# Performance work log

Hardware: AMD Instinct MI355X
Metric: run time of the kernel (lower is better)

The kernel has to match this reference:

```python
import jax, jax.numpy as jnp
import numpy as np


def conv(x, w, b=None, pad=1):
    y = jax.lax.conv_general_dilated(x, w, (1, 1), [(pad, pad), (pad, pad)],
                                     dimension_numbers=('NCHW', 'OIHW', 'NCHW'))
    if b is not None:
        y = y + b[None, :, None, None]
    return y


def grid_sample(img, gx, gy):
    # bilinear, zeros padding, align_corners=False (torch F.grid_sample default)
    B, C, H, W = img.shape
    ix = ((gx + 1.0) * W - 1.0) * 0.5
    iy = ((gy + 1.0) * H - 1.0) * 0.5
    x0 = jnp.floor(ix)
    y0 = jnp.floor(iy)

    def gather(xi, yi):
        valid = (xi >= 0) & (xi <= W - 1) & (yi >= 0) & (yi <= H - 1)
        xc = jnp.clip(xi, 0, W - 1).astype(jnp.int32)
        yc = jnp.clip(yi, 0, H - 1).astype(jnp.int32)
        b = jnp.arange(B)[:, None, None]
        return img[b, :, yc, xc] * valid[..., None].astype(img.dtype)  # (B,H,W,C)

    wx1 = ix - x0
    wy1 = iy - y0
    wx0 = 1.0 - wx1
    wy0 = 1.0 - wy1
    out = (gather(x0, y0) * (wx0 * wy0)[..., None]
           + gather(x0 + 1, y0) * (wx1 * wy0)[..., None]
           + gather(x0, y0 + 1) * (wx0 * wy1)[..., None]
           + gather(x0 + 1, y0 + 1) * (wx1 * wy1)[..., None])
    return out.transpose(0, 3, 1, 2)  # (B,C,H,W)


def setup_inputs() -> dict:
    key = jax.random.key(0)
    ks = jax.random.split(key, 32)
    B, H, W, hd = 4, 512, 512, 16
    f = lambda k, shp: jax.random.normal(k, shp, dtype=jnp.float32) * 0.05
    z = lambda n: jnp.zeros((n,), dtype=jnp.float32)
    d = {
        'net': f(ks[0], (B, hd, H, W)),
        'inp': f(ks[1], (B, hd, H, W)),
        'corr': f(ks[2], (B, 3, H, W)),
        'noise': f(ks[3], (B, 3, H, W)),
        # BasicMotionEncoder (channels=3, hidden=32, output_dim=64)
        'wc1': f(ks[4], (32, 3, 3, 3)), 'bc1': z(32),
        'wc2': f(ks[5], (32, 32, 3, 3)), 'bc2': z(32),
        'wf1': f(ks[6], (32, 3, 3, 3)), 'bf1': z(32),
        'wf2': f(ks[7], (32, 32, 3, 3)), 'bf2': z(32),
        'we': f(ks[8], (61, 64, 3, 3)), 'be': z(61),
        # SepConvGRU (hidden_size=16, L=4)
        'loc1_w': f(ks[9], (16, 96, 5, 5)), 'loc1_b': z(16),
        'loc2_w': f(ks[10], (8, 16, 5, 5)), 'loc2_b': z(8),
        'wz': f(ks[11], (16, 144, 3, 3)), 'bz': z(16),
        'wr': f(ks[12], (16, 144, 3, 3)), 'br': z(16),
        'wq': f(ks[13], (16, 96, 3, 3)), 'bq': z(16),
        # CBAM (reduction 16 -> mid=1; bias-free, standard impl)
        'ca_w1': f(ks[14], (1, 16, 1, 1)),
        'ca_w2': f(ks[15], (16, 1, 1, 1)),
        'sa_w': f(ks[16], (1, 2, 7, 7)),
        # FlowHead (input 16, hidden 64, out 3)
        'fh1_w': f(ks[17], (64, 16, 3, 3)), 'fh1_b': z(64),
        'fh2_w': f(ks[18], (3, 64, 3, 3)), 'fh2_b': z(3),
    }
    return d


def reference(net, inp, corr, noise, wc1, bc1, wc2, bc2, wf1, bf1, wf2, bf2, we, be,
              loc1_w, loc1_b, loc2_w, loc2_b, wz, bz, wr, br, wq, bq,
              ca_w1, ca_w2, sa_w, fh1_w, fh1_b, fh2_w, fh2_b):
    # --- BasicMotionEncoder ---
    cor = jax.nn.relu(conv(corr, wc1, bc1, 1))
    cor = jax.nn.relu(conv(cor, wc2, bc2, 1))
    flo = jax.nn.relu(conv(noise, wf1, bf1, 1))
    flo = jax.nn.relu(conv(flo, wf2, bf2, 1))
    mo = jax.nn.relu(conv(jnp.concatenate([cor, flo], 1), we, be, 1))
    motion = jnp.concatenate([mo, noise], 1)  # (B,64,H,W)
    x = jnp.concatenate([inp, motion], 1)     # (B,hd+64,H,W)
    h = net
    B, C, H, W = h.shape
    # --- SepConvGRU ---
    t = jax.nn.leaky_relu(conv(jnp.concatenate([x, h], 1), loc1_w, loc1_b, 2), 0.2)
    flows = conv(t, loc2_w, loc2_b, 2)        # (B,2L,H,W)
    L = flows.shape[1] // 2
    flows = flows.reshape(B, L, 2, H, W)
    xx = jnp.arange(W, dtype=h.dtype)[None, None, :]  # (1,1,W)
    yy = jnp.arange(H, dtype=h.dtype)[None, :, None]  # (1,H,1)

    def warp_one(flow):  # flow: (B,2,H,W); warp h by -flow
        vgx = xx - flow[:, 0]
        vgy = yy - flow[:, 1]
        gx = 2.0 * vgx / max(W - 1, 1) - 1.0
        gy = 2.0 * vgy / max(H - 1, 1) - 1.0
        return grid_sample(h, gx, gy)

    wrapped = jax.vmap(warp_one, in_axes=1, out_axes=1)(flows)  # (B,L,C,H,W)
    wrapped = wrapped.reshape(B, L * C, H, W)
    hx = jnp.concatenate([wrapped, x], 1)     # (B,9*hd,H,W)
    zg = jax.nn.sigmoid(conv(hx, wz, bz, 1))
    rg = jax.nn.sigmoid(conv(hx, wr, br, 1))
    q = jnp.tanh(conv(jnp.concatenate([rg * h, x], 1), wq, bq, 1))
    h = (1.0 - zg) * h + zg * q
    # --- CBAM ---
    avg = h.mean((2, 3), keepdims=True)
    mx = h.max((2, 3), keepdims=True)
    mlp = lambda v: conv(jax.nn.relu(conv(v, ca_w1, None, 0)), ca_w2, None, 0)
    h = h * jax.nn.sigmoid(mlp(avg) + mlp(mx))
    sa = jnp.concatenate([h.mean(1, keepdims=True), h.max(1, keepdims=True)], 1)
    h = h * jax.nn.sigmoid(conv(sa, sa_w, None, 3))
    # --- FlowHead ---
    delta_flow = conv(jax.nn.relu(conv(h, fh1_w, fh1_b, 1)), fh2_w, fh2_b, 1)
    return h, delta_flow
```

## Files before the change

### kernel.cpp

```cpp
#include <hip/hip_runtime.h>
#include <hip/hip_bf16.h>
#include <math.h>

using bf16 = __hip_bfloat16;
typedef __attribute__((ext_vector_type(8))) short short8;
typedef __attribute__((ext_vector_type(4))) float f32x4;

__device__ __forceinline__ float b2f(bf16 v){ return __bfloat162float(v); }
__device__ __forceinline__ bf16 f2b(float v){ return __float2bfloat16(v); }
__device__ __forceinline__ float bs2f(short s){
  union{unsigned u; float f;} x; x.u = ((unsigned)(unsigned short)s)<<16; return x.f;
}

template<int A> __device__ __forceinline__ float act_fn(float v){
  if constexpr (A==1) return fmaxf(v, 0.f);
  else if constexpr (A==2) return v > 0.f ? v : 0.2f*v;
  else if constexpr (A==3) return 1.f/(1.f+expf(-v));
  else if constexpr (A==4) return tanhf(v);
  else return v;
}

struct Srcs9 { const bf16* p[9]; int code[9]; };

template<int KK, int ACT, int NT>
__global__ __launch_bounds__(256) void conv_mfma(
    Srcs9 S, int Gin, const bf16* __restrict__ flows,
    const bf16* __restrict__ Bw, const float* __restrict__ bias,
    bf16* __restrict__ outS, size_t slabS, float* __restrict__ outF, int Cout,
    int H, int W)
{
  constexpr int TS=16, HALO=TS+KK-1, PAD=KK/2, NPAIR=(KK*KK+1)/2, HH=HALO*HALO;
  constexpr int NMT = (NT==1)?4:((NT==2)?8:16);
  __shared__ __align__(16) bf16 As[2][HH*24];
  const int tid=threadIdx.x, lane=tid&63, wv=tid>>6;
  const int ln=lane&15, gq=lane>>4;
  const int tilesx=W/TS;
  const int tx0=(blockIdx.x%tilesx)*TS, ty0=(blockIdx.x/tilesx)*TS;
  const int b=blockIdx.z; const int HW=H*W;
  int ntile, mt0;
  if constexpr (NT==1){ ntile=0;    mt0=wv*4; }
  else if constexpr (NT==2){ ntile=wv&1; mt0=(wv>>1)*8; }
  else { ntile=wv; mt0=0; }

  f32x4 acc[NMT];
  #pragma unroll
  for (int t=0;t<NMT;++t) acc[t]=(f32x4){0.f,0.f,0.f,0.f};

  const short8 Z8 = {0,0,0,0,0,0,0,0};
  const int px0=tid, px1=tid+256;
  const int hy0=px0/HALO, hx0=px0-hy0*HALO;
  const int hy1=px1/HALO, hx1=px1-hy1*HALO;
  const bool act1 = (px1<HH);
  const int gy0=ty0+hy0-PAD, gx0=tx0+hx0-PAD;
  const int gy1=ty0+hy1-PAD, gx1=tx0+hx1-PAD;
  const bool in0 = (gy0>=0&&gy0<H&&gx0>=0&&gx0<W);
  const bool in1 = act1 && (gy1>=0&&gy1<H&&gx1>=0&&gx1<W);
  const size_t po0 = ((size_t)b*HW + (size_t)(in0?gy0:0)*W + (in0?gx0:0))*16;
  const size_t po1 = ((size_t)b*HW + (size_t)(in1?gy1:0)*W + (in1?gx1:0))*16;

  auto gather = [&](int g, bool inb, size_t po, int gy, int gx, short8& A0, short8& A1){
    const int code = S.code[g];
    const bf16* sp = S.p[g];
    if (code == 0) {
      if (inb) {
        const bf16* qp = sp + po;
        A0 = *(const short8*)qp; A1 = *(const short8*)(qp+8);
      } else { A0 = Z8; A1 = Z8; }
    } else {
      if (inb) {
        const int l = code-1;
        const unsigned fp_ = *(const unsigned*)(flows + po + 2*l);
        const float fx = bs2f((short)(fp_&0xffff)), fy = bs2f((short)(fp_>>16));
        const float vgx = (float)gx - fx, vgy = (float)gy - fy;
        const float gxn = 2.f*vgx/(float)(W-1) - 1.f;
        const float gyn = 2.f*vgy/(float)(H-1) - 1.f;
        const float ix = ((gxn+1.f)*(float)W - 1.f)*0.5f;
        const float iy = ((gyn+1.f)*(float)H - 1.f)*0.5f;
        const float x0f = floorf(ix), y0f = floorf(iy);
        const float wx1 = ix-x0f, wy1 = iy-y0f, wx0 = 1.f-wx1, wy0 = 1.f-wy1;
        const int x0=(int)x0f, y0=(int)y0f, x1=x0+1, y1=y0+1;
        const bool vx0=(x0>=0)&(x0<W), vx1=(x1>=0)&(x1<W);
        const bool vy0=(y0>=0)&(y0<H), vy1=(y1>=0)&(y1<H);
        const int xc0=min(max(x0,0),W-1), xc1=min(max(x1,0),W-1);
        const int yc0=min(max(y0,0),H-1), yc1=min(max(y1,0),H-1);
        const float w00=wx0*wy0*((vx0&&vy0)?1.f:0.f);
        const float w10=wx1*wy0*((vx1&&vy0)?1.f:0.f);
        const float w01=wx0*wy1*((vx0&&vy1)?1.f:0.f);
        const float w11=wx1*wy1*((vx1&&vy1)?1.f:0.f);
        const bf16* nb = sp + (size_t)b*HW*16;
        const bf16* p00 = nb + ((size_t)yc0*W+xc0)*16;
        const bf16* p10 = nb + ((size_t)yc0*W+xc1)*16;
        const bf16* p01 = nb + ((size_t)yc1*W+xc0)*16;
        const bf16* p11 = nb + ((size_t)yc1*W+xc1)*16;
        const short8 a00=*(const short8*)p00, b00=*(const short8*)(p00+8);
        const short8 a10=*(const short8*)p10, b10=*(const short8*)(p10+8);
        const short8 a01=*(const short8*)p01, b01=*(const short8*)(p01+8);
        const short8 a11=*(const short8*)p11, b11=*(const short8*)(p11+8);
        __align__(16) bf16 tmp[16];
        #pragma unroll
        for (int c=0;c<8;++c){
          tmp[c]   = f2b(w00*bs2f(a00[c]) + w10*bs2f(a10[c]) + w01*bs2f(a01[c]) + w11*bs2f(a11[c]));
          tmp[8+c] = f2b(w00*bs2f(b00[c]) + w10*bs2f(b10[c]) + w01*bs2f(b01[c]) + w11*bs2f(b11[c]));
        }
        A0 = *(const short8*)tmp; A1 = *(const short8*)(tmp+8);
      } else { A0 = Z8; A1 = Z8; }
    }
  };

  auto mfma_g = [&](int g, const char* bufc){
    const bf16* bw = Bw + ((size_t)g*NPAIR*NT + ntile)*512;
    const char* bufm = bufc + (size_t)mt0*(HALO*48);
    #pragma unroll
    for (int p=0;p<NPAIR;++p){
      const short8 bfrag = *(const short8*)(bw + (size_t)p*(NT*512) + lane*8);
      int off = 2*p + (gq>>1);
      if (off >= KK*KK) off = 0;
      const int dy = off/KK, dx = off - (off/KK)*KK;
      const int ce = (dy*HALO + ln + dx)*48 + ((gq&1)<<4);
      #pragma unroll
      for (int t=0;t<NMT;++t){
        const short8 af = *(const short8*)(bufm + (size_t)t*(HALO*48) + ce);
        acc[t] = __builtin_amdgcn_mfma_f32_16x16x32_bf16(af, bfrag, acc[t], 0, 0, 0);
      }
    }
  };

  for (int g=0; g<Gin; ++g) {
    short8 a0, a1, c0v, c1v;
    gather(g, in0, po0, gy0, gx0, a0, a1);
    if (act1) gather(g, in1, po1, gy1, gx1, c0v, c1v);
    if (g > 0) mfma_g(g-1, (const char*)As[(g-1)&1]);
    bf16* buf = As[g&1];
    *(short8*)(buf + (size_t)px0*24)     = a0;
    *(short8*)(buf + (size_t)px0*24 + 8) = a1;
    if (act1){
      *(short8*)(buf + (size_t)px1*24)     = c0v;
      *(short8*)(buf + (size_t)px1*24 + 8) = c1v;
    }
    __syncthreads();
  }
  mfma_g(Gin-1, (const char*)As[(Gin-1)&1]);

  const int co = ntile*16 + ln;
  const float bv = bias[co];
  if (outS) {
    #pragma unroll
    for (int t=0;t<NMT;++t){
      const int y = ty0 + mt0 + t;
      bf16* op = outS + (size_t)ntile*slabS + ((size_t)b*HW + (size_t)y*W + tx0 + gq*4)*16 + ln;
      #pragma unroll
      for (int r=0;r<4;++r) op[(size_t)r*16] = f2b(act_fn<ACT>(acc[t][r] + bv));
    }
  } else {
    if (co < Cout) {
      #pragma unroll
      for (int t=0;t<NMT;++t){
        const int y = ty0 + mt0 + t;
        float4 f;
        f.x = act_fn<ACT>(acc[t][0]+bv); f.y = act_fn<ACT>(acc[t][1]+bv);
        f.z = act_fn<ACT>(acc[t][2]+bv); f.w = act_fn<ACT>(acc[t][3]+bv);
        *(float4*)(outF + ((size_t)b*Cout + co)*HW + (size_t)y*W + tx0 + gq*4) = f;
      }
    }
  }
}

struct PrepDesc {
  const float *W1, *W2, *b1, *b2;
  int coSplit, NPAIR, NTp, Cout, CinO, T;
  int lo0, hi0, d2, lo2, hi2;
  int base[9];
  int total;
};
struct PrepAll { PrepDesc d[10]; int n; };

__global__ void prep_w(PrepAll P, bf16* __restrict__ Bw, float* __restrict__ bOut, int grand){
  const int i = blockIdx.x*256 + threadIdx.x;
  if (i < P.n*64) {
    const int c=i>>6, t=i&63; const PrepDesc& D=P.d[c];
    float bv=0.f;
    if (t < D.Cout) bv = (!D.b2 || t < D.coSplit) ? D.b1[t] : D.b2[t-D.coSplit];
    bOut[c*64+t]=bv;
  }
  if (i >= grand) return;
  int c=0, off0=0;
  while (i >= off0 + P.d[c].total) { off0 += P.d[c].total; ++c; }
  const PrepDesc& D = P.d[c];
  const int j = i - off0;
  const int jj=j&7, l=(j>>3)&63, ln2=l&15, gq2=l>>4;
  int r=j>>9; const int nt=r%D.NTp; r/=D.NTp; const int p=r%D.NPAIR; const int g=r/D.NPAIR;
  const int k=gq2*8+jj, off=2*p+(k>>4), ci=k&15, co=nt*16+ln2;
  float w=0.f;
  if (off<D.T && co<D.Cout) {
    const int lo = (g==0)?D.lo0:0, hi=(g==0)?D.hi0:16;
    if (!D.W2 || co < D.coSplit) {
      if (ci>=lo && ci<hi) w = D.W1[((size_t)co*D.CinO + D.base[g]+ci)*D.T + off];
    } else {
      if (ci>=D.lo2 && ci<D.hi2) w = D.W2[((size_t)(co-D.coSplit)*D.CinO + D.base[g]+ci+D.d2)*D.T + off];
    }
  }
  Bw[i] = f2b(w);
}

__global__ void pack_all(const float* __restrict__ corr, const float* __restrict__ noise,
                         const float* __restrict__ inp, const float* __restrict__ net,
                         bf16* __restrict__ cnoise, bf16* __restrict__ inpT,
                         bf16* __restrict__ netT, int HW){
  const int px = blockIdx.x*256+threadIdx.x; const int b=blockIdx.y;
  if (px>=HW) return;
  const size_t base = ((size_t)b*HW+px)*16;
  __align__(16) bf16 t[16];
  #pragma unroll
  for (int c=0;c<16;++c) t[c]=f2b(0.f);
  #pragma unroll
  for (int c=0;c<3;++c){
    t[c]   = f2b(corr [((size_t)b*3+c)*HW+px]);
    t[3+c] = f2b(noise[((size_t)b*3+c)*HW+px]);
  }
  *(short8*)(cnoise+base) = *(const short8*)t; *(short8*)(cnoise+base+8) = *(const short8*)(t+8);
  #pragma unroll
  for (int c=0;c<16;++c) t[c]=f2b(inp[((size_t)b*16+c)*HW+px]);
  *(short8*)(inpT+base) = *(const short8*)t; *(short8*)(inpT+base+8) = *(const short8*)(t+8);
  #pragma unroll
  for (int c=0;c<16;++c) t[c]=f2b(net[((size_t)b*16+c)*HW+px]);
  *(short8*)(netT+base) = *(const short8*)t; *(short8*)(netT+base+8) = *(const short8*)(t+8);
}

__global__ void noise_tail(const float* __restrict__ noise, bf16* __restrict__ mslab3, int HW){
  const int px = blockIdx.x*256+threadIdx.x; const int b=blockIdx.y;
  if (px>=HW) return;
  bf16* d = mslab3 + ((size_t)b*HW+px)*16;
  #pragma unroll
  for (int c=0;c<3;++c) d[13+c] = f2b(noise[((size_t)b*3+c)*HW+px]);
}

__global__ void rh_k(const bf16* __restrict__ rg, const bf16* __restrict__ netT,
                     bf16* __restrict__ rh, int HW){
  const int px = blockIdx.x*256+threadIdx.x; const int b=blockIdx.y;
  if (px>=HW) return;
  const size_t base = ((size_t)b*HW+px)*16;
  const short8 r0=*(const short8*)(rg+base),  r1=*(const short8*)(rg+base+8);
  const short8 n0=*(const short8*)(netT+base), n1=*(const short8*)(netT+base+8);
  __align__(16) bf16 t[16];
  #pragma unroll
  for (int c=0;c<8;++c){
    t[c]   = f2b(bs2f(r0[c])*bs2f(n0[c]));
    t[8+c] = f2b(bs2f(r1[c])*bs2f(n1[c]));
  }
  *(short8*)(rh+base) = *(const short8*)t; *(short8*)(rh+base+8) = *(const short8*)(t+8);
}

__global__ void h1_k(const bf16* __restrict__ zg, const bf16* __restrict__ q,
                     const float* __restrict__ net, bf16* __restrict__ hT, int HW){
  const int px = blockIdx.x*256+threadIdx.x; const int b=blockIdx.y;
  if (px>=HW) return;
  const size_t base = ((size_t)b*HW+px)*16;
  const short8 z0=*(const short8*)(zg+base), z1=*(const short8*)(zg+base+8);
  const short8 q0=*(const short8*)(q+base),  q1=*(const short8*)(q+base+8);
  __align__(16) bf16 t[16];
  #pragma unroll
  for (int c=0;c<8;++c){
    const float za=bs2f(z0[c]), zb=bs2f(z1[c]);
    const float na=net[((size_t)b*16+c)*HW+px], nb2=net[((size_t)b*16+8+c)*HW+px];
    t[c]   = f2b((1.f-za)*na + za*bs2f(q0[c]));
    t[8+c] = f2b((1.f-zb)*nb2 + zb*bs2f(q1[c]));
  }
  *(short8*)(hT+base) = *(const short8*)t; *(short8*)(hT+base+8) = *(const short8*)(t+8);
}

__global__ __launch_bounds__(256) void castats_p1(const bf16* __restrict__ hT,
                                                  float* __restrict__ part, int HW){
  const int blk=blockIdx.x, b=blockIdx.y;
  const int per = HW>>5;
  const bf16* base = hT + ((size_t)b*HW + (size_t)blk*per)*16;
  float s[16], m[16];
  #pragma unroll
  for (int c=0;c<16;++c){ s[c]=0.f; m[c]=-3.4e38f; }
  for (int i=threadIdx.x;i<per;i+=256){
    const short8 a=*(const short8*)(base+(size_t)i*16);
    const short8 bb=*(const short8*)(base+(size_t)i*16+8);
    #pragma unroll
    for (int c=0;c<8;++c){
      const float v=bs2f(a[c]);  s[c]+=v;   m[c]=fmaxf(m[c],v);
      const float w=bs2f(bb[c]); s[8+c]+=w; m[8+c]=fmaxf(m[8+c],w);
    }
  }
  #pragma unroll
  for (int o=32;o>=1;o>>=1){
    #pragma unroll
    for (int c=0;c<16;++c){ s[c]+=__shfl_down(s[c],o); m[c]=fmaxf(m[c],__shfl_down(m[c],o)); }
  }
  __shared__ float ls[4][16], lm[4][16];
  const int w4=threadIdx.x>>6;
  if ((threadIdx.x&63)==0){
    #pragma unroll
    for (int c=0;c<16;++c){ ls[w4][c]=s[c]; lm[w4][c]=m[c]; }
  }
  __syncthreads();
  if (threadIdx.x<16){
    const int c=threadIdx.x;
    part[((size_t)(b*32+blk))*32 + c]      = ls[0][c]+ls[1][c]+ls[2][c]+ls[3][c];
    part[((size_t)(b*32+blk))*32 + 16 + c] = fmaxf(fmaxf(lm[0][c],lm[1][c]),fmaxf(lm[2][c],lm[3][c]));
  }
}

__global__ void castats_fin(const float* __restrict__ part, const float* __restrict__ w1,
                            const float* __restrict__ w2, float* __restrict__ scale, int HW){
  const int t = threadIdx.x; if (t>=64) return;
  const int b=t>>4, c=t&15;
  float s=0.f, m=-3.4e38f;
  for (int k=0;k<32;++k){
    s += part[((size_t)(b*32+k))*32 + c];
    m  = fmaxf(m, part[((size_t)(b*32+k))*32 + 16 + c]);
  }
  float pa = w1[c]*(s/(float)HW), pm = w1[c]*m;
  #pragma unroll
  for (int o=8;o>=1;o>>=1){ pa += __shfl_xor(pa,o,16); pm += __shfl_xor(pm,o,16); }
  const float y = w2[c]*fmaxf(pa,0.f) + w2[c]*fmaxf(pm,0.f);
  scale[t] = 1.f/(1.f+expf(-y));
}

__global__ void sastats_k(const bf16* __restrict__ hT, const float* __restrict__ scale,
                          bf16* __restrict__ sa2, int HW){
  const int px = blockIdx.x*256+threadIdx.x; const int b=blockIdx.y;
  if (px>=HW) return;
  const size_t base = ((size_t)b*HW+px)*16;
  const short8 a=*(const short8*)(hT+base), c8=*(const short8*)(hT+base+8);
  float s=0.f, m=-3.4e38f;
  #pragma unroll
  for (int c=0;c<8;++c){
    const float v=bs2f(a[c])*scale[b*16+c];    s+=v; m=fmaxf(m,v);
    const float w=bs2f(c8[c])*scale[b*16+8+c]; s+=w; m=fmaxf(m,w);
  }
  sa2[((size_t)b*2+0)*HW+px] = f2b(s*(1.f/16.f));
  sa2[((size_t)b*2+1)*HW+px] = f2b(m);
}

__global__ __launch_bounds__(256) void hfinal2(bf16* __restrict__ hT, const float* __restrict__ scale,
    const bf16* __restrict__ sa2, const float* __restrict__ saw,
    float* __restrict__ outh, int H, int W){
  __shared__ float wl[98];
  if (threadIdx.x < 98) wl[threadIdx.x] = saw[threadIdx.x];
  __syncthreads();
  const int i = blockIdx.x*256 + threadIdx.x; const int b = blockIdx.y;
  const int HW = H*W;
  if (i >= HW) return;
  const int y = i / W, x = i - (i/W)*W;
  float s = 0.f;
  #pragma unroll
  for (int ch=0; ch<2; ++ch){
    const size_t base = ((size_t)b*2+ch)*HW;
    for (int ky=0;ky<7;++ky){
      const int yy=y+ky-3; if (yy<0||yy>=H) continue;
      for (int kx=0;kx<7;++kx){
        const int xx=x+kx-3; if (xx<0||xx>=W) continue;
        s += b2f(sa2[base+(size_t)yy*W+xx]) * wl[ch*49+ky*7+kx];
      }
    }
  }
  const float sa = 1.f/(1.f+expf(-s));
  const size_t base = ((size_t)b*HW+i)*16;
  const short8 a=*(const short8*)(hT+base), c8=*(const short8*)(hT+base+8);
  __align__(16) bf16 t[16];
  #pragma unroll
  for (int c=0;c<8;++c){
    const float v=bs2f(a[c])*scale[b*16+c]*sa;
    const float w=bs2f(c8[c])*scale[b*16+8+c]*sa;
    t[c]=f2b(v); t[8+c]=f2b(w);
    outh[((size_t)b*16+c)*HW+i]=v; outh[((size_t)b*16+8+c)*HW+i]=w;
  }
  *(short8*)(hT+base)=*(const short8*)t; *(short8*)(hT+base+8)=*(const short8*)(t+8);
}

extern "C" void kernel_launch(void* const* d_in, const int* in_sizes, int n_in,
                              void* d_out, int out_size, void* d_ws, size_t ws_size,
                              hipStream_t stream)
{
  const float* net   = (const float*)d_in[0];
  const float* inp   = (const float*)d_in[1];
  const float* corr  = (const float*)d_in[2];
  const float* noise = (const float*)d_in[3];
  const float* wc1 = (const float*)d_in[4];  const float* bc1 = (const float*)d_in[5];
  const float* wc2 = (const float*)d_in[6];  const float* bc2 = (const float*)d_in[7];
  const float* wf1 = (const float*)d_in[8];  const float* bf1 = (const float*)d_in[9];
  const float* wf2 = (const float*)d_in[10]; const float* bf2 = (const float*)d_in[11];
  const float* we  = (const float*)d_in[12]; const float* be  = (const float*)d_in[13];
  const float* loc1_w = (const float*)d_in[14]; const float* loc1_b = (const float*)d_in[15];
  const float* loc2_w = (const float*)d_in[16]; const float* loc2_b = (const float*)d_in[17];
  const float* wz = (const float*)d_in[18]; const float* bz = (const float*)d_in[19];
  const float* wr = (const float*)d_in[20]; const float* br = (const float*)d_in[21];
  const float* wq = (const float*)d_in[22]; const float* bq = (const float*)d_in[23];
  const float* ca_w1 = (const float*)d_in[24]; const float* ca_w2 = (const float*)d_in[25];
  const float* sa_w  = (const float*)d_in[26];
  const float* fh1_w = (const float*)d_in[27]; const float* fh1_b = (const float*)d_in[28];
  const float* fh2_w = (const float*)d_in[29]; const float* fh2_b = (const float*)d_in[30];

  const int B = 4, H = 512, W = 512, HW = H*W;
  const size_t U  = 32ull<<20;
  const size_t SS = (size_t)B*HW*16;
  char* ws = (char*)d_ws;

  bf16* cor1   = (bf16*)(ws + 0*U);
  bf16* flo1   = (bf16*)(ws + 2*U);
  bf16* motion = (bf16*)(ws + 0*U);
  bf16* fh1o   = (bf16*)(ws + 0*U);
  bf16* inpT   = (bf16*)(ws + 4*U);
  bf16* flo2   = (bf16*)(ws + 5*U);
  bf16* flows  = (bf16*)(ws + 5*U);
  bf16* qb     = (bf16*)(ws + 5*U);
  bf16* cnoise = (bf16*)(ws + 6*U);
  bf16* tbuf   = (bf16*)(ws + 6*U);
  bf16* rh     = (bf16*)(ws + 6*U);
  bf16* hT     = (bf16*)(ws + 6*U);
  bf16* netT   = (bf16*)(ws + 7*U);
  float* part    = (float*)(ws + 4*U);
  float* scale   = (float*)(ws + 4*U + (64<<10));
  bf16*  sa2     = (bf16*)(ws + 4*U + (1<<20));
  bf16*  Bw_fh2  = (bf16*)(ws + 4*U + (16<<20));
  float* bias_fh2= (float*)(ws + 4*U + (17<<20));

  float* out_h  = (float*)d_out;
  float* out_df = out_h + (size_t)B*16*HW;
  bf16*  zgrg   = (bf16*)d_out;
  bf16*  BwAll  = (bf16*)out_df;
  float* biasAll= (float*)(BwAll + 190464);

  const size_t oMrg=0, oCor2=10240, oFlo2=20480, oMo=30720, oLoc1=71680,
               oLoc2=111616, oZgrg=118272, oQ=164352, oFh1=179712;
  const int grand = 189952;

  const dim3 pgrid((HW+255)/256, B);
  const dim3 cgrid((W/16)*(H/16), 1, B);

  auto mk = [](const float* W1, const float* W2, int coSplit, const float* b1, const float* b2,
               int G, int NP, int NTp, int Cout, int CinO, int T,
               int lo0, int hi0, int d2, int lo2, int hi2,
               int b0,int b1_,int b2_,int b3,int b4,int b5,int b6,int b7,int b8)->PrepDesc{
    PrepDesc d{};
    d.W1=W1; d.W2=W2; d.b1=b1; d.b2=b2; d.coSplit=coSplit;
    d.NPAIR=NP; d.NTp=NTp; d.Cout=Cout; d.CinO=CinO; d.T=T;
    d.lo0=lo0; d.hi0=hi0; d.d2=d2; d.lo2=lo2; d.hi2=hi2;
    const int bs[9]={b0,b1_,b2_,b3,b4,b5,b6,b7,b8};
    for (int g=0;g<9;++g) d.base[g]=bs[g];
    d.total = G*NP*NTp*512;
    return d;
  };

  {
    PrepAll P{}; P.n = 9;
    P.d[0] = mk(wc1, wf1, 32, bc1, bf1, 1,5,4, 64,3,9,  0,3, -3,3,6, 0,0,0,0,0,0,0,0,0);
    P.d[1] = mk(wc2, nullptr,0, bc2,nullptr, 2,5,2, 32,32,9, 0,16, 0,0,16, 0,16,0,0,0,0,0,0,0);
    P.d[2] = mk(wf2, nullptr,0, bf2,nullptr, 2,5,2, 32,32,9, 0,16, 0,0,16, 0,16,0,0,0,0,0,0,0);
    P.d[3] = mk(we,  nullptr,0, be, nullptr, 4,5,4, 61,64,9, 0,16, 0,0,16, 0,16,32,48,0,0,0,0,0);
    P.d[4] = mk(loc1_w,nullptr,0, loc1_b,nullptr, 6,13,1, 16,96,25, 0,16, 0,0,16, 0,16,32,48,64,80,0,0,0);
    P.d[5] = mk(loc2_w,nullptr,0, loc2_b,nullptr, 1,13,1, 8,16,25,  0,16, 0,0,16, 0,0,0,0,0,0,0,0,0);
    P.d[6] = mk(wz, wr, 16, bz, br, 9,5,2, 32,144,9, 0,16, 0,0,16, 0,16,32,48,64,80,96,112,128);
    P.d[7] = mk(wq, nullptr,0, bq, nullptr, 6,5,1, 16,96,9, 0,16, 0,0,16, 0,16,32,48,64,80,0,0,0);
    P.d[8] = mk(fh1_w,nullptr,0, fh1_b,nullptr, 1,5,4, 64,16,9, 0,16, 0,0,16, 0,0,0,0,0,0,0,0,0);
    prep_w<<<(grand+255)/256,256,0,stream>>>(P, BwAll, biasAll, grand);
  }

  pack_all<<<pgrid,256,0,stream>>>(corr, noise, inp, net, cnoise, inpT, netT, HW);

  { Srcs9 S{}; S.p[0]=cnoise;
    conv_mfma<3,1,4><<<cgrid,256,0,stream>>>(S,1,nullptr,BwAll+oMrg,biasAll+0*64,cor1,SS,nullptr,64,H,W); }
  { Srcs9 S{}; S.p[0]=cor1; S.p[1]=cor1+SS;
    conv_mfma<3,1,2><<<cgrid,256,0,stream>>>(S,2,nullptr,BwAll+oCor2,biasAll+1*64,zgrg,SS,nullptr,32,H,W); }
  { Srcs9 S{}; S.p[0]=flo1; S.p[1]=flo1+SS;
    conv_mfma<3,1,2><<<cgrid,256,0,stream>>>(S,2,nullptr,BwAll+oFlo2,biasAll+2*64,flo2,SS,nullptr,32,H,W); }
  { Srcs9 S{}; S.p[0]=zgrg; S.p[1]=zgrg+SS; S.p[2]=flo2; S.p[3]=flo2+SS;
    conv_mfma<3,1,4><<<cgrid,256,0,stream>>>(S,4,nullptr,BwAll+oMo,biasAll+3*64,motion,SS,nullptr,61,H,W); }
  noise_tail<<<pgrid,256,0,stream>>>(noise, motion+3*SS, HW);

  { Srcs9 S{}; S.p[0]=inpT; S.p[1]=motion; S.p[2]=motion+SS; S.p[3]=motion+2*SS; S.p[4]=motion+3*SS; S.p[5]=netT;
    conv_mfma<5,2,1><<<cgrid,256,0,stream>>>(S,6,nullptr,BwAll+oLoc1,biasAll+4*64,tbuf,SS,nullptr,16,H,W); }
  { Srcs9 S{}; S.p[0]=tbuf;
    conv_mfma<5,0,1><<<cgrid,256,0,stream>>>(S,1,nullptr,BwAll+oLoc2,biasAll+5*64,flows,SS,nullptr,8,H,W); }

  { Srcs9 S{};
    S.p[0]=netT; S.code[0]=1; S.p[1]=netT; S.code[1]=2;
    S.p[2]=netT; S.code[2]=3; S.p[3]=netT; S.code[3]=4;
    S.p[4]=inpT; S.p[5]=motion; S.p[6]=motion+SS; S.p[7]=motion+2*SS; S.p[8]=motion+3*SS;
    conv_mfma<3,3,2><<<cgrid,256,0,stream>>>(S,9,flows,BwAll+oZgrg,biasAll+6*64,zgrg,SS,nullptr,32,H,W); }
  rh_k<<<pgrid,256,0,stream>>>(zgrg+SS, netT, rh, HW);
  { Srcs9 S{}; S.p[0]=rh; S.p[1]=inpT; S.p[2]=motion; S.p[3]=motion+SS; S.p[4]=motion+2*SS; S.p[5]=motion+3*SS;
    conv_mfma<3,4,1><<<cgrid,256,0,stream>>>(S,6,nullptr,BwAll+oQ,biasAll+7*64,qb,SS,nullptr,16,H,W); }
  h1_k<<<pgrid,256,0,stream>>>(zgrg, qb, net, hT, HW);

  { PrepAll P{}; P.n = 1;
    P.d[0] = mk(fh2_w,nullptr,0, fh2_b,nullptr, 4,5,1, 3,64,9, 0,16, 0,0,16, 0,16,32,48,0,0,0,0,0);
    prep_w<<<(10240+255)/256,256,0,stream>>>(P, Bw_fh2, bias_fh2, 10240); }

  castats_p1<<<dim3(32,B),256,0,stream>>>(hT, part, HW);
  castats_fin<<<1,64,0,stream>>>(part, ca_w1, ca_w2, scale, HW);
  sastats_k<<<pgrid,256,0,stream>>>(hT, scale, sa2, HW);
  hfinal2<<<pgrid,256,0,stream>>>(hT, scale, sa2, sa_w, out_h, H, W);

  { Srcs9 S{}; S.p[0]=hT;
    conv_mfma<3,1,4><<<cgrid,256,0,stream>>>(S,1,nullptr,BwAll+oFh1,biasAll+8*64,fh1o,SS,nullptr,64,H,W); }
  { Srcs9 S{}; S.p[0]=fh1o; S.p[1]=fh1o+SS; S.p[2]=fh1o+2*SS; S.p[3]=fh1o+3*SS;
    conv_mfma<3,0,1><<<cgrid,256,0,stream>>>(S,4,nullptr,Bw_fh2,bias_fh2,nullptr,SS,out_df,3,H,W); }
}
```

Measured before the change: 993.9 us.

## Compute all output-channel tiles per wave and pad LDS pixel stride

Each wave now handles four output rows across all NT output-channel tiles, instead of splitting channel tiles across waves. Each A fragment loaded from LDS is then reused across NT MFMAs, which cuts LDS reads. The LDS per-pixel stride also grows from 24 to 28 bf16 elements, likely to reduce bank conflicts. In exchange, accumulator registers grow with NT (up to 4x4 f32x4), each wave loads more B fragments, and occupancy may fall.

```diff
diff --git a/kernel.cpp b/kernel.cpp
--- a/kernel.cpp
+++ b/kernel.cpp
@@ -30,21 +30,20 @@
     int H, int W)
 {
   constexpr int TS=16, HALO=TS+KK-1, PAD=KK/2, NPAIR=(KK*KK+1)/2, HH=HALO*HALO;
-  constexpr int NMT = (NT==1)?4:((NT==2)?8:16);
-  __shared__ __align__(16) bf16 As[2][HH*24];
+  constexpr int CP=28, CPB=56;
+  __shared__ __align__(16) bf16 As[2][HH*CP];
   const int tid=threadIdx.x, lane=tid&63, wv=tid>>6;
   const int ln=lane&15, gq=lane>>4;
   const int tilesx=W/TS;
   const int tx0=(blockIdx.x%tilesx)*TS, ty0=(blockIdx.x/tilesx)*TS;
   const int b=blockIdx.z; const int HW=H*W;
-  int ntile, mt0;
-  if constexpr (NT==1){ ntile=0;    mt0=wv*4; }
-  else if constexpr (NT==2){ ntile=wv&1; mt0=(wv>>1)*8; }
-  else { ntile=wv; mt0=0; }
-
-  f32x4 acc[NMT];
-  #pragma unroll
-  for (int t=0;t<NMT;++t) acc[t]=(f32x4){0.f,0.f,0.f,0.f};
+  const int mt0 = wv*4;
+
+  f32x4 acc[4][NT];
+  #pragma unroll
+  for (int t=0;t<4;++t)
+    #pragma unroll
+    for (int n=0;n<NT;++n) acc[t][n]=(f32x4){0.f,0.f,0.f,0.f};
 
   const short8 Z8 = {0,0,0,0,0,0,0,0};
   const int px0=tid, px1=tid+256;
@@ -108,19 +107,24 @@
   };
 
   auto mfma_g = [&](int g, const char* bufc){
-    const bf16* bw = Bw + ((size_t)g*NPAIR*NT + ntile)*512;
-    const char* bufm = bufc + (size_t)mt0*(HALO*48);
+    const bf16* bw = Bw + (size_t)g*NPAIR*NT*512;
+    const char* bufm = bufc + (size_t)mt0*(HALO*CPB);
     #pragma unroll
     for (int p=0;p<NPAIR;++p){
-      const short8 bfrag = *(const short8*)(bw + (size_t)p*(NT*512) + lane*8);
+      short8 bfrag[NT];
+      #pragma unroll
+      for (int n=0;n<NT;++n)
+        bfrag[n] = *(const short8*)(bw + ((size_t)p*NT+n)*512 + lane*8);
       int off = 2*p + (gq>>1);
       if (off >= KK*KK) off = 0;
       const int dy = off/KK, dx = off - (off/KK)*KK;
-      const int ce = (dy*HALO + ln + dx)*48 + ((gq&1)<<4);
+      const int ce = (dy*HALO + ln + dx)*CPB + ((gq&1)<<4);
       #pragma unroll
-      for (int t=0;t<NMT;++t){
-        const short8 af = *(const short8*)(bufm + (size_t)t*(HALO*48) + ce);
-        acc[t] = __builtin_amdgcn_mfma_f32_16x16x32_bf16(af, bfrag, acc[t], 0, 0, 0);
+      for (int t=0;t<4;++t){
+        const short8 af = *(const short8*)(bufm + (size_t)t*(HALO*CPB) + ce);
+        #pragma unroll
+        for (int n=0;n<NT;++n)
+          acc[t][n] = __builtin_amdgcn_mfma_f32_16x16x32_bf16(af, bfrag[n], acc[t][n], 0, 0, 0);
       }
     }
   };
@@ -131,35 +135,38 @@
     if (act1) gather(g, in1, po1, gy1, gx1, c0v, c1v);
     if (g > 0) mfma_g(g-1, (const char*)As[(g-1)&1]);
     bf16* buf = As[g&1];
-    *(short8*)(buf + (size_t)px0*24)     = a0;
-    *(short8*)(buf + (size_t)px0*24 + 8) = a1;
+    *(short8*)(buf + (size_t)px0*CP)     = a0;
+    *(short8*)(buf + (size_t)px0*CP + 8) = a1;
     if (act1){
-      *(short8*)(buf + (size_t)px1*24)     = c0v;
-      *(short8*)(buf + (size_t)px1*24 + 8) = c1v;
+      *(short8*)(buf + (size_t)px1*CP)     = c0v;
+      *(short8*)(buf + (size_t)px1*CP + 8) = c1v;
     }
     __syncthreads();
   }
   mfma_g(Gin-1, (const char*)As[(Gin-1)&1]);
 
-  const int co = ntile*16 + ln;
-  const float bv = bias[co];
-  if (outS) {
-    #pragma unroll
-    for (int t=0;t<NMT;++t){
-      const int y = ty0 + mt0 + t;
-      bf16* op = outS + (size_t)ntile*slabS + ((size_t)b*HW + (size_t)y*W + tx0 + gq*4)*16 + ln;
+  #pragma unroll
+  for (int n=0;n<NT;++n){
+    const int co = n*16 + ln;
+    const float bv = bias[co];
+    if (outS) {
       #pragma unroll
-      for (int r=0;r<4;++r) op[(size_t)r*16] = f2b(act_fn<ACT>(acc[t][r] + bv));
-    }
-  } else {
-    if (co < Cout) {
-      #pragma unroll
-      for (int t=0;t<NMT;++t){
+      for (int t=0;t<4;++t){
         const int y = ty0 + mt0 + t;
-        float4 f;
-        f.x = act_fn<ACT>(acc[t][0]+bv); f.y = act_fn<ACT>(acc[t][1]+bv);
-        f.z = act_fn<ACT>(acc[t][2]+bv); f.w = act_fn<ACT>(acc[t][3]+bv);
-        *(float4*)(outF + ((size_t)b*Cout + co)*HW + (size_t)y*W + tx0 + gq*4) = f;
+        bf16* op = outS + (size_t)n*slabS + ((size_t)b*HW + (size_t)y*W + tx0 + gq*4)*16 + ln;
+        #pragma unroll
+        for (int r=0;r<4;++r) op[(size_t)r*16] = f2b(act_fn<ACT>(acc[t][n][r] + bv));
+      }
+    } else {
+      if (co < Cout) {
+        #pragma unroll
+        for (int t=0;t<4;++t){
+          const int y = ty0 + mt0 + t;
+          float4 f;
+          f.x = act_fn<ACT>(acc[t][n][0]+bv); f.y = act_fn<ACT>(acc[t][n][1]+bv);
+          f.z = act_fn<ACT>(acc[t][n][2]+bv); f.w = act_fn<ACT>(acc[t][n][3]+bv);
+          *(float4*)(outF + ((size_t)b*Cout + co)*HW + (size_t)y*W + tx0 + gq*4) = f;
+        }
       }
     }
   }
```

Result: slower. 2.266 ms (+128.0%).
